# Optimization experiments

Hardware: AMD Instinct MI355X
Metric: run time of the kernel (lower is better)

## Reference

```python
import jax, jax.numpy as jnp
import numpy as np

N, E, F, H, G, C, L = 50000, 800000, 128, 256, 128, 10, 3


def _gcn(x, src, dst, norm, W, b, n):
    # PyG GCNConv: h = x W; out_i = sum_{j->i} norm_ji h_j (+ self loops already in src/dst); + bias
    h = x @ W
    msg = h[src] * norm[:, None]              # [E+N, H]
    return jax.ops.segment_sum(msg, dst, num_segments=n) + b


def setup_inputs() -> dict:
    key = jax.random.key(0)
    ks = jax.random.split(key, 8)
    x = jax.random.normal(ks[0], (N, F), dtype=jnp.float32)
    edge_index = jax.random.randint(ks[1], (2, E), 0, N, dtype=jnp.int32)
    batch = jnp.sort(jax.random.randint(ks[2], (N,), 0, G, dtype=jnp.int32))
    graph_hidden = jax.random.normal(ks[3], (G, H), dtype=jnp.float32)
    W0 = jax.random.normal(ks[4], (F, H), dtype=jnp.float32) / np.sqrt(F)
    b0 = jnp.zeros((H,), jnp.float32)
    Ws = jax.random.normal(ks[5], (L, H, H), dtype=jnp.float32) / np.sqrt(H)
    bs = jnp.zeros((L, H), jnp.float32)
    Wlin = jax.random.normal(ks[6], (H, C), dtype=jnp.float32) / np.sqrt(H)
    blin = jnp.zeros((C,), jnp.float32)
    return {"x": x, "edge_index": edge_index, "batch": batch, "graph_hidden": graph_hidden,
            "W0": W0, "b0": b0, "Ws": Ws, "bs": bs, "Wlin": Wlin, "blin": blin}


def reference(x, edge_index, batch, graph_hidden, W0, b0, Ws, bs, Wlin, blin):
    n = x.shape[0]
    loops = jnp.arange(n, dtype=edge_index.dtype)
    src = jnp.concatenate([edge_index[0], loops])   # self loops appended
    dst = jnp.concatenate([edge_index[1], loops])
    deg = jax.ops.segment_sum(jnp.ones_like(src, dtype=x.dtype), dst, num_segments=n)
    inv_sqrt = jnp.where(deg > 0, jax.lax.rsqrt(deg), 0.0)
    norm = inv_sqrt[src] * inv_sqrt[dst]            # [E+N]

    h = _gcn(x, src, dst, norm, W0, b0, n)          # to_hidden (no activation, matches source)
    res = jax.lax.stop_gradient(graph_hidden[batch])  # no_grad residual, vectorized
    for i in range(Ws.shape[0]):
        h = h + res
        h = jax.nn.relu(_gcn(h, src, dst, norm, Ws[i], bs[i], n))
        # dropout is identity in eval mode

    counts = jax.ops.segment_sum(jnp.ones((n,), x.dtype), batch, num_segments=G)
    gm = jax.ops.segment_sum(h, batch, num_segments=G) / jnp.maximum(counts, 1.0)[:, None]
    gm = gm + graph_hidden
    y = gm @ Wlin + blin
    return (y, gm)
```

## Files before the change

### kernel.cpp

```cpp
#include <hip/hip_runtime.h>


typedef __bf16 bf16x8 __attribute__((ext_vector_type(8)));
typedef float f32x4 __attribute__((ext_vector_type(4)));
typedef float f32x2 __attribute__((ext_vector_type(2)));

__device__ inline float bf2f(unsigned short u) {
  union { unsigned int i; float f; } v;
  v.i = (unsigned int)u << 16;
  return v.f;
}
__device__ inline unsigned short f2bf(float f) {
  union { unsigned int i; float f; } v;
  v.f = f;
  unsigned int i = v.i;
  return (unsigned short)((i + 0x7fffu + ((i >> 16) & 1u)) >> 16);
}
__device__ inline unsigned int pack2(float a, float b) {
  return (unsigned int)f2bf(a) | ((unsigned int)f2bf(b) << 16);
}
__device__ inline void acc8(float* acc, uint4 r) {
  unsigned int w[4] = {r.x, r.y, r.z, r.w};
#pragma unroll
  for (int q = 0; q < 4; ++q) {
    acc[2 * q] += bf2f((unsigned short)(w[q] & 0xffffu));
    acc[2 * q + 1] += bf2f((unsigned short)(w[q] >> 16));
  }
}
__device__ inline unsigned pack4_fp8(float a, float b, float c, float d) {
  int r = 0;
  r = __builtin_amdgcn_cvt_pk_fp8_f32(a, b, r, false);
  r = __builtin_amdgcn_cvt_pk_fp8_f32(c, d, r, true);
  return (unsigned)r;
}
__device__ inline void acc16_fp8(float* acc, uint4 r, unsigned msk) {
  unsigned w[4] = {r.x, r.y, r.z, r.w};
#pragma unroll
  for (int d = 0; d < 4; ++d) {
    int v = (int)(w[d] & msk);
    f32x2 lo = __builtin_amdgcn_cvt_pk_f32_fp8(v, false);
    f32x2 hi = __builtin_amdgcn_cvt_pk_f32_fp8(v, true);
    acc[4 * d + 0] += lo[0];
    acc[4 * d + 1] += lo[1];
    acc[4 * d + 2] += hi[0];
    acc[4 * d + 3] += hi[1];
  }
}


__global__ void count_pos_kernel(const int* __restrict__ dst, int* __restrict__ deg,
                                 unsigned short* __restrict__ pos, int E) {
  int e = blockIdx.x * blockDim.x + threadIdx.x;
  if (e < E) pos[e] = (unsigned short)atomicAdd(&deg[dst[e]], 1);
}

__global__ void scan_partial_kernel(const int* __restrict__ deg, float* __restrict__ inv_s,
                                    int* __restrict__ bsum, int N) {
  __shared__ int s[256];
  int i = blockIdx.x * 256 + threadIdx.x;
  int d = (i < N) ? deg[i] : 0;
  if (i < N) inv_s[i] = rsqrtf((float)(d + 1));
  s[threadIdx.x] = d;
  __syncthreads();
  for (int off = 128; off > 0; off >>= 1) {
    if (threadIdx.x < off) s[threadIdx.x] += s[threadIdx.x + off];
    __syncthreads();
  }
  if (threadIdx.x == 0) bsum[blockIdx.x] = s[0];
}

__global__ void scan_block_kernel(const int* __restrict__ bsum, int* __restrict__ boff,
                                  int* __restrict__ row_off, int NB, int N) {
  __shared__ int s[256];
  int v = (threadIdx.x < NB) ? bsum[threadIdx.x] : 0;
  s[threadIdx.x] = v;
  __syncthreads();
  for (int off = 1; off < 256; off <<= 1) {
    int t = (threadIdx.x >= off) ? s[threadIdx.x - off] : 0;
    __syncthreads();
    s[threadIdx.x] += t;
    __syncthreads();
  }
  boff[threadIdx.x] = s[threadIdx.x] - v;
  if (threadIdx.x == 255) row_off[N] = s[255];
}

__global__ void scan_final_kernel(const int* __restrict__ deg, const int* __restrict__ boff,
                                  int* __restrict__ row_off, int N) {
  __shared__ int s[256];
  int i = blockIdx.x * 256 + threadIdx.x;
  int v = (i < N) ? deg[i] : 0;
  s[threadIdx.x] = v;
  __syncthreads();
  for (int off = 1; off < 256; off <<= 1) {
    int t = (threadIdx.x >= off) ? s[threadIdx.x - off] : 0;
    __syncthreads();
    s[threadIdx.x] += t;
    __syncthreads();
  }
  if (i < N) row_off[i] = boff[blockIdx.x] + s[threadIdx.x] - v;
}

__global__ void fill_csr2_kernel(const int* __restrict__ src, const int* __restrict__ dst,
                                 const unsigned short* __restrict__ pos,
                                 const int* __restrict__ row_off, int* __restrict__ col, int E) {
  int t = blockIdx.x * blockDim.x + threadIdx.x;
  int e = t * 4;
  if (e + 3 < E) {
    int4 s4 = *(const int4*)&src[e];
    int4 d4 = *(const int4*)&dst[e];
    ushort4 p4 = *(const ushort4*)&pos[e];
    col[row_off[d4.x] + p4.x] = s4.x;
    col[row_off[d4.y] + p4.y] = s4.y;
    col[row_off[d4.z] + p4.z] = s4.z;
    col[row_off[d4.w] + p4.w] = s4.w;
  } else {
    for (; e < E; ++e) col[row_off[dst[e]] + pos[e]] = src[e];
  }
}

__global__ void prep_all_kernel(const float* __restrict__ x, const float* __restrict__ inv_s,
                                unsigned* __restrict__ u, int total_dw,
                                const float* __restrict__ W0, const float* __restrict__ Ws,
                                unsigned short* __restrict__ Wt0,
                                unsigned short* __restrict__ WtS) {
  const int FH = 128 * 256, HH = 256 * 256;
  int idx = blockIdx.x * 256 + threadIdx.x;
  if (idx < total_dw) {
    int i = idx >> 5;
    float s = inv_s[i];
    float4 v = *(const float4*)&x[(size_t)idx * 4];
    u[idx] = pack4_fp8(s * v.x, s * v.y, s * v.z, s * v.w);
  } else {
    int w = idx - total_dw;
    if (w < FH) {
      int k = w >> 8, n = w & 255;
      Wt0[n * 128 + k] = f2bf(W0[w]);
    } else {
      int t = w - FH;
      if (t < 3 * HH) {
        int l = t >> 16;
        int rem = t & 65535;
        int k = rem >> 8, n = rem & 255;
        WtS[l * HH + n * 256 + k] = f2bf(Ws[t]);
      }
    }
  }
}

template <int CH>
__global__ __launch_bounds__(256) void aggregate_fp8_kernel(
    const unsigned char* __restrict__ u, const int* __restrict__ row_off,
    const int* __restrict__ col, const float* __restrict__ inv_s,
    unsigned short* __restrict__ out, int N) {
  constexpr int LPR = CH / 16;
  constexpr int EPW = 64 / LPR;
  int wave = threadIdx.x >> 6;
  int lane = threadIdx.x & 63;
  int i = blockIdx.x * 4 + wave;
  if (i >= N) return;
  int sub = lane / LPR;
  int c = lane % LPR;
  int e0 = row_off[i], e1 = row_off[i + 1];
  int last = e1 - 1;
  float acc[16] = {};
  for (int e = e0 + sub; e < e1; e += 4 * EPW) {
    unsigned off[4];
    unsigned msk[4];
#pragma unroll
    for (int q = 0; q < 4; ++q) {
      int ee = e + q * EPW;
      bool v = ee < e1;
      int j = col[v ? ee : last];
      off[q] = (unsigned)j * CH + c * 16;
      msk[q] = v ? 0xffffffffu : 0u;
    }
    uint4 r[4];
#pragma unroll
    for (int q = 0; q < 4; ++q) r[q] = *(const uint4*)(u + off[q]);
#pragma unroll
    for (int q = 0; q < 4; ++q) acc16_fp8(acc, r[q], msk[q]);
  }
#pragma unroll
  for (int o = 32; o >= LPR; o >>= 1)
#pragma unroll
    for (int k = 0; k < 16; ++k) acc[k] += __shfl_down(acc[k], o);
  if (lane < LPR) {
    uint4 self = *(const uint4*)(u + (size_t)i * CH + c * 16);
    acc16_fp8(acc, self, 0xffffffffu);
    float s = inv_s[i];
    uint4 o1, o2;
    o1.x = pack2(s * acc[0], s * acc[1]);
    o1.y = pack2(s * acc[2], s * acc[3]);
    o1.z = pack2(s * acc[4], s * acc[5]);
    o1.w = pack2(s * acc[6], s * acc[7]);
    o2.x = pack2(s * acc[8], s * acc[9]);
    o2.y = pack2(s * acc[10], s * acc[11]);
    o2.z = pack2(s * acc[12], s * acc[13]);
    o2.w = pack2(s * acc[14], s * acc[15]);
    *(uint4*)&out[(size_t)i * CH + c * 16] = o1;
    *(uint4*)&out[(size_t)i * CH + c * 16 + 8] = o2;
  }
}

template <int K, bool RELU, bool WRITE_U>
__global__ __launch_bounds__(512) void gemm_kernel(
    const unsigned short* __restrict__ A,
    const unsigned short* __restrict__ Bt,
    const float* __restrict__ bias,
    const float* __restrict__ inv_s, const int* __restrict__ batch,
    const float* __restrict__ gh,
    void* __restrict__ outp,
    int M) {
  constexpr int BK = 32;
  constexpr int LDT = 40;
  __shared__ unsigned short As[128 * LDT];
  __shared__ unsigned short Bs[256 * LDT];
  int tid = threadIdx.x;
  int wave = tid >> 6, lane = tid & 63;
  int quad = lane >> 4, l15 = lane & 15;
  int wr = wave >> 2, wc = wave & 3;
  int row0 = blockIdx.x * 128;
  f32x4 acc[4][4];
#pragma unroll
  for (int m = 0; m < 4; ++m)
#pragma unroll
    for (int n = 0; n < 4; ++n) acc[m][n] = (f32x4){0.f, 0.f, 0.f, 0.f};

  for (int k0 = 0; k0 < K; k0 += BK) {
    {
      int r = tid >> 2, kq = tid & 3;
      int gr = row0 + r;
      uint4 v = make_uint4(0u, 0u, 0u, 0u);
      if (gr < M) v = *(const uint4*)&A[(size_t)gr * K + k0 + kq * 8];
      *(uint4*)&As[r * LDT + kq * 8] = v;
    }
#pragma unroll
    for (int p = 0; p < 2; ++p) {
      int n = (tid >> 2) + p * 128, kq = tid & 3;
      *(uint4*)&Bs[n * LDT + kq * 8] = *(const uint4*)&Bt[(size_t)n * K + k0 + kq * 8];
    }
    __syncthreads();
    bf16x8 af[4], bfr[4];
#pragma unroll
    for (int m = 0; m < 4; ++m)
      af[m] = __builtin_bit_cast(
          bf16x8, *(const uint4*)&As[(wr * 64 + m * 16 + l15) * LDT + quad * 8]);
#pragma unroll
    for (int n = 0; n < 4; ++n)
      bfr[n] = __builtin_bit_cast(
          bf16x8, *(const uint4*)&Bs[(wc * 64 + n * 16 + l15) * LDT + quad * 8]);
#pragma unroll
    for (int m = 0; m < 4; ++m)
#pragma unroll
      for (int n = 0; n < 4; ++n)
        acc[m][n] = __builtin_amdgcn_mfma_f32_16x16x32_bf16(af[m], bfr[n], acc[m][n], 0, 0, 0);
    __syncthreads();
  }
#pragma unroll
  for (int m = 0; m < 4; ++m) {
#pragma unroll
    for (int r = 0; r < 4; ++r) {
      int gr = row0 + wr * 64 + m * 16 + quad * 4 + r;
      if (gr >= M) continue;
      float sv = 1.0f;
      int bofs = 0;
      if (WRITE_U) {
        sv = inv_s[gr];
        bofs = batch[gr] * 256;
      }
#pragma unroll
      for (int n = 0; n < 4; ++n) {
        int cc = wc * 64 + n * 16 + l15;
        float v = acc[m][n][r] + bias[cc];
        if (RELU) v = fmaxf(v, 0.f);
        if (WRITE_U) {
          v = sv * (v + gh[bofs + cc]);
          unsigned pr = (unsigned)__builtin_amdgcn_cvt_pk_fp8_f32(v, v, 0, false);
          ((unsigned char*)outp)[(size_t)gr * 256 + cc] = (unsigned char)(pr & 0xffu);
        } else {
          ((unsigned short*)outp)[(size_t)gr * 256 + cc] = f2bf(v);
        }
      }
    }
  }
}


__global__ void pool_kernel(const unsigned short* __restrict__ h, const int* __restrict__ batch,
                            float* __restrict__ gmsum, float* __restrict__ cnt, int N, int chunk) {
  int start = blockIdx.x * chunk;
  int end = min(start + chunk, N);
  if (start >= end) return;
  int c = threadIdx.x;
  int g = batch[start];
  float acc = 0.0f;
  int run = 0;
  for (int n = start; n < end; ++n) {
    int bg = batch[n];
    if (bg != g) {
      atomicAdd(&gmsum[g * 256 + c], acc);
      if (c == 0) atomicAdd(&cnt[g], (float)run);
      acc = 0.0f;
      run = 0;
      g = bg;
    }
    acc += bf2f(h[(size_t)n * 256 + c]);
    run++;
  }
  atomicAdd(&gmsum[g * 256 + c], acc);
  if (c == 0) atomicAdd(&cnt[g], (float)run);
}

__global__ void final_kernel(const float* __restrict__ gmsum, const float* __restrict__ cnt,
                             const float* __restrict__ gh, const float* __restrict__ Wlin,
                             const float* __restrict__ blin, float* __restrict__ y,
                             float* __restrict__ gm_out, int G) {
  int g = blockIdx.x;
  int c = threadIdx.x;
  __shared__ float row[256];
  float v = gmsum[g * 256 + c] / fmaxf(cnt[g], 1.0f) + gh[g * 256 + c];
  gm_out[g * 256 + c] = v;
  row[c] = v;
  __syncthreads();
  if (c < 10) {
    float acc = blin[c];
    for (int k = 0; k < 256; ++k) acc += row[k] * Wlin[k * 10 + c];
    y[g * 10 + c] = acc;
  }
}


extern "C" void kernel_launch(void* const* d_in, const int* in_sizes, int n_in,
                              void* d_out, int out_size, void* d_ws, size_t ws_size,
                              hipStream_t stream) {
  const float* x = (const float*)d_in[0];
  const int* ei = (const int*)d_in[1];
  const int* batch = (const int*)d_in[2];
  const float* gh = (const float*)d_in[3];
  const float* W0 = (const float*)d_in[4];
  const float* b0 = (const float*)d_in[5];
  const float* Ws = (const float*)d_in[6];
  const float* bs = (const float*)d_in[7];
  const float* Wlin = (const float*)d_in[8];
  const float* blin = (const float*)d_in[9];
  float* out = (float*)d_out;

  const int N = in_sizes[2];
  const int E = in_sizes[1] / 2;
  const int G = in_sizes[3] / 256;
  const int H = 256, L = 3, C = 10, F = 128;

  char* ws = (char*)d_ws;
  size_t off = 0;
  auto alloc = [&](size_t bytes) {
    void* p = ws + off;
    off += (bytes + 255) & ~(size_t)255;
    return p;
  };
  size_t cntspan = ((size_t)G * 4 + 255) & ~(size_t)255;
  int* deg = (int*)alloc((size_t)N * 4);
  float* cnt = (float*)alloc((size_t)G * 4);
  float* gmsum = (float*)alloc((size_t)G * H * 4);
  int* row_off = (int*)alloc((size_t)(N + 1) * 4);
  int* bsum = (int*)alloc(256 * 4);
  int* boff = (int*)alloc(256 * 4);
  int* col = (int*)alloc((size_t)E * 4);
  unsigned short* pos = (unsigned short*)alloc((size_t)E * 2);
  float* inv_s = (float*)alloc((size_t)N * 4);
  unsigned char* u_x = (unsigned char*)alloc((size_t)N * F);
  unsigned char* uA = (unsigned char*)alloc((size_t)N * H);
  unsigned short* aggA = (unsigned short*)alloc((size_t)N * H * 2);
  unsigned short* hfin = (unsigned short*)alloc((size_t)N * H * 2);
  unsigned short* Wt0 = (unsigned short*)alloc((size_t)F * H * 2);
  unsigned short* WtS = (unsigned short*)alloc((size_t)L * H * H * 2);

  const int* srcv = ei;
  const int* dstv = ei + E;

  hipMemsetAsync(deg, 0, (size_t)N * 4, stream);
  hipMemsetAsync(cnt, 0, cntspan + (size_t)G * H * 4, stream);

  int EB = (E + 255) / 256;
  int NB = (N + 255) / 256;
  count_pos_kernel<<<EB, 256, 0, stream>>>(dstv, deg, pos, E);
  scan_partial_kernel<<<NB, 256, 0, stream>>>(deg, inv_s, bsum, N);
  scan_block_kernel<<<1, 256, 0, stream>>>(bsum, boff, row_off, NB, N);
  scan_final_kernel<<<NB, 256, 0, stream>>>(deg, boff, row_off, N);
  fill_csr2_kernel<<<(E / 4 + 256) / 256 + 1, 256, 0, stream>>>(srcv, dstv, pos, row_off, col, E);

  int UXDW = N * (F / 4);
  int TW = F * H + 3 * H * H;
  prep_all_kernel<<<(UXDW + TW + 255) / 256, 256, 0, stream>>>(x, inv_s, (unsigned*)u_x, UXDW,
                                                               W0, Ws, Wt0, WtS);

  int AGG_GRID = (N + 3) / 4;
  int GEMM_GRID = (N + 127) / 128;

  aggregate_fp8_kernel<128><<<AGG_GRID, 256, 0, stream>>>(u_x, row_off, col, inv_s, aggA, N);
  gemm_kernel<128, false, true><<<GEMM_GRID, 512, 0, stream>>>(aggA, Wt0, b0, inv_s, batch, gh,
                                                               uA, N);
  for (int l = 0; l < 2; ++l) {
    aggregate_fp8_kernel<256><<<AGG_GRID, 256, 0, stream>>>(uA, row_off, col, inv_s, aggA, N);
    gemm_kernel<256, true, true><<<GEMM_GRID, 512, 0, stream>>>(
        aggA, WtS + (size_t)l * H * H, bs + (size_t)l * H, inv_s, batch, gh, uA, N);
  }
  aggregate_fp8_kernel<256><<<AGG_GRID, 256, 0, stream>>>(uA, row_off, col, inv_s, aggA, N);
  gemm_kernel<256, true, false><<<GEMM_GRID, 512, 0, stream>>>(
      aggA, WtS + (size_t)2 * H * H, bs + (size_t)2 * H, inv_s, batch, gh, hfin, N);

  int PB = 1024;
  int chunk = (N + PB - 1) / PB;
  pool_kernel<<<PB, 256, 0, stream>>>(hfin, batch, gmsum, cnt, N, chunk);
  final_kernel<<<G, 256, 0, stream>>>(gmsum, cnt, gh, Wlin, blin, out, out + (size_t)G * C, G);
}
```

Before: 395.8 us.

## Fuse pooling into last GEMM, merge CSR fill with prep, slice 256-wide aggregation

```diff
diff --git a/kernel.cpp b/kernel.cpp
--- a/kernel.cpp
+++ b/kernel.cpp
@@ -18,14 +18,6 @@
 }
 __device__ inline unsigned int pack2(float a, float b) {
   return (unsigned int)f2bf(a) | ((unsigned int)f2bf(b) << 16);
-}
-__device__ inline void acc8(float* acc, uint4 r) {
-  unsigned int w[4] = {r.x, r.y, r.z, r.w};
-#pragma unroll
-  for (int q = 0; q < 4; ++q) {
-    acc[2 * q] += bf2f((unsigned short)(w[q] & 0xffffu));
-    acc[2 * q + 1] += bf2f((unsigned short)(w[q] >> 16));
-  }
 }
 __device__ inline unsigned pack4_fp8(float a, float b, float c, float d) {
   int r = 0;
@@ -45,6 +37,14 @@
     acc[4 * d + 2] += hi[0];
     acc[4 * d + 3] += hi[1];
   }
+}
+__device__ inline int lbound(const int* a, int n, int key) {
+  int lo = 0, hi = n;
+  while (lo < hi) {
+    int mid = (lo + hi) >> 1;
+    if (a[mid] < key) lo = mid + 1; else hi = mid;
+  }
+  return lo;
 }
 
 
@@ -101,48 +101,50 @@
   if (i < N) row_off[i] = boff[blockIdx.x] + s[threadIdx.x] - v;
 }
 
-__global__ void fill_csr2_kernel(const int* __restrict__ src, const int* __restrict__ dst,
+__global__ void fill_prep_kernel(const int* __restrict__ src, const int* __restrict__ dst,
                                  const unsigned short* __restrict__ pos,
-                                 const int* __restrict__ row_off, int* __restrict__ col, int E) {
-  int t = blockIdx.x * blockDim.x + threadIdx.x;
-  int e = t * 4;
-  if (e + 3 < E) {
-    int4 s4 = *(const int4*)&src[e];
-    int4 d4 = *(const int4*)&dst[e];
-    ushort4 p4 = *(const ushort4*)&pos[e];
-    col[row_off[d4.x] + p4.x] = s4.x;
-    col[row_off[d4.y] + p4.y] = s4.y;
-    col[row_off[d4.z] + p4.z] = s4.z;
-    col[row_off[d4.w] + p4.w] = s4.w;
+                                 const int* __restrict__ row_off, int* __restrict__ col, int E,
+                                 int FB, const float* __restrict__ x,
+                                 const float* __restrict__ inv_s, unsigned* __restrict__ u,
+                                 int total_dw, const float* __restrict__ W0,
+                                 const float* __restrict__ Ws, unsigned short* __restrict__ Wt0,
+                                 unsigned short* __restrict__ WtS) {
+  const int FH = 128 * 256, HH = 256 * 256;
+  int b = blockIdx.x;
+  if (b < FB) {
+    int t = b * 256 + threadIdx.x;
+    int e = t * 4;
+    if (e + 3 < E) {
+      int4 s4 = *(const int4*)&src[e];
+      int4 d4 = *(const int4*)&dst[e];
+      ushort4 p4 = *(const ushort4*)&pos[e];
+      col[row_off[d4.x] + p4.x] = s4.x;
+      col[row_off[d4.y] + p4.y] = s4.y;
+      col[row_off[d4.z] + p4.z] = s4.z;
+      col[row_off[d4.w] + p4.w] = s4.w;
+    } else {
+      for (; e < E; ++e) col[row_off[dst[e]] + pos[e]] = src[e];
+    }
   } else {
-    for (; e < E; ++e) col[row_off[dst[e]] + pos[e]] = src[e];
-  }
-}
-
-__global__ void prep_all_kernel(const float* __restrict__ x, const float* __restrict__ inv_s,
-                                unsigned* __restrict__ u, int total_dw,
-                                const float* __restrict__ W0, const float* __restrict__ Ws,
-                                unsigned short* __restrict__ Wt0,
-                                unsigned short* __restrict__ WtS) {
-  const int FH = 128 * 256, HH = 256 * 256;
-  int idx = blockIdx.x * 256 + threadIdx.x;
-  if (idx < total_dw) {
-    int i = idx >> 5;
-    float s = inv_s[i];
-    float4 v = *(const float4*)&x[(size_t)idx * 4];
-    u[idx] = pack4_fp8(s * v.x, s * v.y, s * v.z, s * v.w);
-  } else {
-    int w = idx - total_dw;
-    if (w < FH) {
-      int k = w >> 8, n = w & 255;
-      Wt0[n * 128 + k] = f2bf(W0[w]);
+    int idx = (b - FB) * 256 + threadIdx.x;
+    if (idx < total_dw) {
+      int i = idx >> 5;
+      float s = inv_s[i];
+      float4 v = *(const float4*)&x[(size_t)idx * 4];
+      u[idx] = pack4_fp8(s * v.x, s * v.y, s * v.z, s * v.w);
     } else {
-      int t = w - FH;
-      if (t < 3 * HH) {
-        int l = t >> 16;
-        int rem = t & 65535;
-        int k = rem >> 8, n = rem & 255;
-        WtS[l * HH + n * 256 + k] = f2bf(Ws[t]);
+      int w = idx - total_dw;
+      if (w < FH) {
+        int k = w >> 8, n = w & 255;
+        Wt0[n * 128 + k] = f2bf(W0[w]);
+      } else {
+        int t2 = w - FH;
+        if (t2 < 3 * HH) {
+          int l = t2 >> 16;
+          int rem = t2 & 65535;
+          int k = rem >> 8, n = rem & 255;
+          WtS[l * HH + n * 256 + k] = f2bf(Ws[t2]);
+        }
       }
     }
   }
@@ -203,7 +205,65 @@
   }
 }
 
-template <int K, bool RELU, bool WRITE_U>
+__global__ __launch_bounds__(256) void aggregate_fp8_sliced_kernel(
+    const unsigned char* __restrict__ u, const int* __restrict__ row_off,
+    const int* __restrict__ col, const float* __restrict__ inv_s,
+    unsigned short* __restrict__ out, int N) {
+  constexpr int CH = 256;
+  constexpr int LPR = 8;
+  constexpr int EPW = 8;
+  int slice = blockIdx.x & 1;
+  int ng = blockIdx.x >> 1;
+  int wave = threadIdx.x >> 6;
+  int lane = threadIdx.x & 63;
+  int i = ng * 4 + wave;
+  if (i >= N) return;
+  int sub = lane / LPR;
+  int c = lane & (LPR - 1);
+  int e0 = row_off[i], e1 = row_off[i + 1];
+  int last = e1 - 1;
+  unsigned sofs = (unsigned)slice * 128 + c * 16;
+  float acc[16] = {};
+  for (int e = e0 + sub; e < e1; e += 4 * EPW) {
+    unsigned off[4];
+    unsigned msk[4];
+#pragma unroll
+    for (int q = 0; q < 4; ++q) {
+      int ee = e + q * EPW;
+      bool v = ee < e1;
+      int j = col[v ? ee : last];
+      off[q] = (unsigned)j * CH + sofs;
+      msk[q] = v ? 0xffffffffu : 0u;
+    }
+    uint4 r[4];
+#pragma unroll
+    for (int q = 0; q < 4; ++q) r[q] = *(const uint4*)(u + off[q]);
+#pragma unroll
+    for (int q = 0; q < 4; ++q) acc16_fp8(acc, r[q], msk[q]);
+  }
+#pragma unroll
+  for (int o = 32; o >= LPR; o >>= 1)
+#pragma unroll
+    for (int k = 0; k < 16; ++k) acc[k] += __shfl_down(acc[k], o);
+  if (lane < LPR) {
+    uint4 self = *(const uint4*)(u + (size_t)i * CH + sofs);
+    acc16_fp8(acc, self, 0xffffffffu);
+    float s = inv_s[i];
+    uint4 o1, o2;
+    o1.x = pack2(s * acc[0], s * acc[1]);
+    o1.y = pack2(s * acc[2], s * acc[3]);
+    o1.z = pack2(s * acc[4], s * acc[5]);
+    o1.w = pack2(s * acc[6], s * acc[7]);
+    o2.x = pack2(s * acc[8], s * acc[9]);
+    o2.y = pack2(s * acc[10], s * acc[11]);
+    o2.z = pack2(s * acc[12], s * acc[13]);
+    o2.w = pack2(s * acc[14], s * acc[15]);
+    *(uint4*)&out[(size_t)i * 256 + slice * 128 + c * 16] = o1;
+    *(uint4*)&out[(size_t)i * 256 + slice * 128 + c * 16 + 8] = o2;
+  }
+}
+
+template <int K, bool RELU, int OUTMODE>
 __global__ __launch_bounds__(512) void gemm_kernel(
     const unsigned short* __restrict__ A,
     const unsigned short* __restrict__ Bt,
@@ -257,69 +317,76 @@
         acc[m][n] = __builtin_amdgcn_mfma_f32_16x16x32_bf16(af[m], bfr[n], acc[m][n], 0, 0, 0);
     __syncthreads();
   }
-#pragma unroll
-  for (int m = 0; m < 4; ++m) {
-#pragma unroll
-    for (int r = 0; r < 4; ++r) {
-      int gr = row0 + wr * 64 + m * 16 + quad * 4 + r;
-      if (gr >= M) continue;
-      float sv = 1.0f;
-      int bofs = 0;
-      if (WRITE_U) {
-        sv = inv_s[gr];
-        bofs = batch[gr] * 256;
-      }
-#pragma unroll
-      for (int n = 0; n < 4; ++n) {
-        int cc = wc * 64 + n * 16 + l15;
-        float v = acc[m][n][r] + bias[cc];
-        if (RELU) v = fmaxf(v, 0.f);
-        if (WRITE_U) {
+  if (OUTMODE == 1) {
+#pragma unroll
+    for (int m = 0; m < 4; ++m) {
+#pragma unroll
+      for (int r = 0; r < 4; ++r) {
+        int gr = row0 + wr * 64 + m * 16 + quad * 4 + r;
+        if (gr >= M) continue;
+        float sv = inv_s[gr];
+        int bofs = batch[gr] * 256;
+#pragma unroll
+        for (int n = 0; n < 4; ++n) {
+          int cc = wc * 64 + n * 16 + l15;
+          float v = acc[m][n][r] + bias[cc];
+          if (RELU) v = fmaxf(v, 0.f);
           v = sv * (v + gh[bofs + cc]);
           unsigned pr = (unsigned)__builtin_amdgcn_cvt_pk_fp8_f32(v, v, 0, false);
           ((unsigned char*)outp)[(size_t)gr * 256 + cc] = (unsigned char)(pr & 0xffu);
-        } else {
-          ((unsigned short*)outp)[(size_t)gr * 256 + cc] = f2bf(v);
         }
       }
     }
-  }
-}
-
-
-__global__ void pool_kernel(const unsigned short* __restrict__ h, const int* __restrict__ batch,
-                            float* __restrict__ gmsum, float* __restrict__ cnt, int N, int chunk) {
-  int start = blockIdx.x * chunk;
-  int end = min(start + chunk, N);
-  if (start >= end) return;
-  int c = threadIdx.x;
-  int g = batch[start];
-  float acc = 0.0f;
-  int run = 0;
-  for (int n = start; n < end; ++n) {
-    int bg = batch[n];
-    if (bg != g) {
-      atomicAdd(&gmsum[g * 256 + c], acc);
-      if (c == 0) atomicAdd(&cnt[g], (float)run);
-      acc = 0.0f;
-      run = 0;
-      g = bg;
-    }
-    acc += bf2f(h[(size_t)n * 256 + c]);
-    run++;
-  }
-  atomicAdd(&gmsum[g * 256 + c], acc);
-  if (c == 0) atomicAdd(&cnt[g], (float)run);
-}
-
-__global__ void final_kernel(const float* __restrict__ gmsum, const float* __restrict__ cnt,
-                             const float* __restrict__ gh, const float* __restrict__ Wlin,
-                             const float* __restrict__ blin, float* __restrict__ y,
-                             float* __restrict__ gm_out, int G) {
+  } else {
+    float* gmsum = (float*)outp;
+    float psum[4] = {0.f, 0.f, 0.f, 0.f};
+    int cur_b = -1;
+#pragma unroll
+    for (int m = 0; m < 4; ++m) {
+#pragma unroll
+      for (int r = 0; r < 4; ++r) {
+        int gr = row0 + wr * 64 + m * 16 + quad * 4 + r;
+        if (gr >= M) continue;
+        int b = batch[gr] * 256;
+        if (b != cur_b) {
+          if (cur_b >= 0) {
+#pragma unroll
+            for (int n = 0; n < 4; ++n)
+              atomicAdd(&gmsum[cur_b + wc * 64 + n * 16 + l15], psum[n]);
+          }
+          cur_b = b;
+#pragma unroll
+          for (int n = 0; n < 4; ++n) psum[n] = 0.f;
+        }
+#pragma unroll
+        for (int n = 0; n < 4; ++n) {
+          int cc = wc * 64 + n * 16 + l15;
+          float v = acc[m][n][r] + bias[cc];
+          if (RELU) v = fmaxf(v, 0.f);
+          psum[n] += v;
+        }
+      }
+    }
+    if (cur_b >= 0) {
+#pragma unroll
+      for (int n = 0; n < 4; ++n)
+        atomicAdd(&gmsum[cur_b + wc * 64 + n * 16 + l15], psum[n]);
+    }
+  }
+}
+
+
+__global__ void final_kernel(const float* __restrict__ gmsum, const int* __restrict__ batch,
+                             int N, const float* __restrict__ gh,
+                             const float* __restrict__ Wlin, const float* __restrict__ blin,
+                             float* __restrict__ y, float* __restrict__ gm_out, int G) {
   int g = blockIdx.x;
   int c = threadIdx.x;
   __shared__ float row[256];
-  float v = gmsum[g * 256 + c] / fmaxf(cnt[g], 1.0f) + gh[g * 256 + c];
+  __shared__ int cnt_s;
+  if (c == 0) cnt_s = lbound(batch, N, g + 1) - lbound(batch, N, g);
+  __syncthreads();
+  float v = gmsum[g * 256 + c] / fmaxf((float)cnt_s, 1.0f) + gh[g * 256 + c];
   gm_out[g * 256 + c] = v;
   row[c] = v;
   __syncthreads();
@@ -358,9 +425,7 @@
     off += (bytes + 255) & ~(size_t)255;
     return p;
   };
-  size_t cntspan = ((size_t)G * 4 + 255) & ~(size_t)255;
   int* deg = (int*)alloc((size_t)N * 4);
-  float* cnt = (float*)alloc((size_t)G * 4);
   float* gmsum = (float*)alloc((size_t)G * H * 4);
   int* row_off = (int*)alloc((size_t)(N + 1) * 4);
   int* bsum = (int*)alloc(256 * 4);
@@ -371,7 +436,6 @@
   unsigned char* u_x = (unsigned char*)alloc((size_t)N * F);
   unsigned char* uA = (unsigned char*)alloc((size_t)N * H);
   unsigned short* aggA = (unsigned short*)alloc((size_t)N * H * 2);
-  unsigned short* hfin = (unsigned short*)alloc((size_t)N * H * 2);
   unsigned short* Wt0 = (unsigned short*)alloc((size_t)F * H * 2);
   unsigned short* WtS = (unsigned short*)alloc((size_t)L * H * H * 2);
 
@@ -379,7 +443,7 @@
   const int* dstv = ei + E;
 
   hipMemsetAsync(deg, 0, (size_t)N * 4, stream);
-  hipMemsetAsync(cnt, 0, cntspan + (size_t)G * H * 4, stream);
+  hipMemsetAsync(gmsum, 0, (size_t)G * H * 4, stream);
 
   int EB = (E + 255) / 256;
   int NB = (N + 255) / 256;
@@ -387,30 +451,32 @@
   scan_partial_kernel<<<NB, 256, 0, stream>>>(deg, inv_s, bsum, N);
   scan_block_kernel<<<1, 256, 0, stream>>>(bsum, boff, row_off, NB, N);
   scan_final_kernel<<<NB, 256, 0, stream>>>(deg, boff, row_off, N);
-  fill_csr2_kernel<<<(E / 4 + 256) / 256 + 1, 256, 0, stream>>>(srcv, dstv, pos, row_off, col, E);
-
+
+  int FB = ((E + 3) / 4 + 255) / 256;
   int UXDW = N * (F / 4);
   int TW = F * H + 3 * H * H;
-  prep_all_kernel<<<(UXDW + TW + 255) / 256, 256, 0, stream>>>(x, inv_s, (unsigned*)u_x, UXDW,
-                                                               W0, Ws, Wt0, WtS);
+  int PREPB = (UXDW + TW + 255) / 256;
+  fill_prep_kernel<<<FB + PREPB, 256, 0, stream>>>(srcv, dstv, pos, row_off, col, E, FB, x,
+                                                   inv_s, (unsigned*)u_x, UXDW, W0, Ws, Wt0,
+                                                   WtS);
 
   int AGG_GRID = (N + 3) / 4;
   int GEMM_GRID = (N + 127) / 128;
 
   aggregate_fp8_kernel<128><<<AGG_GRID, 256, 0, stream>>>(u_x, row_off, col, inv_s, aggA, N);
-  gemm_kernel<128, false, true><<<GEMM_GRID, 512, 0, stream>>>(aggA, Wt0, b0, inv_s, batch, gh,
-                                                               uA, N);
+  gemm_kernel<128, false, 1><<<GEMM_GRID, 512, 0, stream>>>(aggA, Wt0, b0, inv_s, batch, gh,
+                                                            uA, N);
   for (int l = 0; l < 2; ++l) {
-    aggregate_fp8_kernel<256><<<AGG_GRID, 256, 0, stream>>>(uA, row_off, col, inv_s, aggA, N);
-    gemm_kernel<256, true, true><<<GEMM_GRID, 512, 0, stream>>>(
+    aggregate_fp8_sliced_kernel<<<AGG_GRID * 2, 256, 0, stream>>>(uA, row_off, col, inv_s, aggA,
+                                                                  N);
+    gemm_kernel<256, true, 1><<<GEMM_GRID, 512, 0, stream>>>(
         aggA, WtS + (size_t)l * H * H, bs + (size_t)l * H, inv_s, batch, gh, uA, N);
   }
-  aggregate_fp8_kernel<256><<<AGG_GRID, 256, 0, stream>>>(uA, row_off, col, inv_s, aggA, N);
-  gemm_kernel<256, true, false><<<GEMM_GRID, 512, 0, stream>>>(
-      aggA, WtS + (size_t)2 * H * H, bs + (size_t)2 * H, inv_s, batch, gh, hfin, N);
-
-  int PB = 1024;
-  int chunk = (N + PB - 1) / PB;
-  pool_kernel<<<PB, 256, 0, stream>>>(hfin, batch, gmsum, cnt, N, chunk);
-  final_kernel<<<G, 256, 0, stream>>>(gmsum, cnt, gh, Wlin, blin, out, out + (size_t)G * C, G);
-}
+  aggregate_fp8_sliced_kernel<<<AGG_GRID * 2, 256, 0, stream>>>(uA, row_off, col, inv_s, aggA,
+                                                                N);
+  gemm_kernel<256, true, 2><<<GEMM_GRID, 512, 0, stream>>>(
+      aggA, WtS + (size_t)2 * H * H, bs + (size_t)2 * H, inv_s, batch, gh, gmsum, N);
+
+  final_kernel<<<G, 256, 0, stream>>>(gmsum, batch, N, gh, Wlin, blin, out,
+                                      out + (size_t)G * C, G);
+}
```

Measured after the change: 447.8 us. 13.1% more time.
